# Kernel optimization log

Measured on AMD Instinct MI355X. Metric: run time of the kernel, lower is better.

The kernel has to match this reference:

```python
import jax, jax.numpy as jnp
import numpy as np

T = 512      # sequence length
D = 256      # char input dim
H = 512      # hidden dim
E = 256      # word embedding dim
V = 100000   # word alphabet size
KC = 2       # max skip-cells consumed per step
KP = 2       # max words starting per step
M = 340      # total lattice matches


def _build_gaz():
    # Deterministic lattice: at every 3rd position, two matched words of lengths 2 and 4.
    rng = np.random.default_rng(0)
    prod_word = np.zeros((T, KP), np.int32)
    prod_dest = np.full((T, KP), M, np.int32)   # default -> dummy slot
    prod_mask = np.zeros((T, KP), np.int32)
    cons_idx = np.zeros((T, KC), np.int32)
    cons_mask = np.zeros((T, KC), np.int32)
    cnt = np.zeros(T, np.int64)
    m = 0
    for t in range(0, T, 3):
        if t + 3 >= T:
            break
        for k, L in enumerate((2, 4)):
            e = t + L - 1  # end position where this word's cell is consumed
            prod_word[t, k] = rng.integers(0, V)
            prod_dest[t, k] = m
            prod_mask[t, k] = 1
            cons_idx[e, cnt[e]] = m
            cons_mask[e, cnt[e]] = 1
            cnt[e] += 1
            m += 1
    assert m == M
    return prod_word, prod_dest, prod_mask, cons_idx, cons_mask


def setup_inputs() -> dict:
    key = jax.random.key(0)
    ks = jax.random.split(key, 10)
    pw, pd, pm, ci, cm = _build_gaz()
    s = jnp.float32(0.05)
    return {
        "x": jax.random.normal(ks[0], (1, T, D), jnp.float32),
        "emb": jax.random.normal(ks[1], (V, E), jnp.float32) * s,
        "weight_ih": jax.random.normal(ks[2], (D, 3 * H), jnp.float32) * s,
        "weight_hh": jax.random.normal(ks[3], (H, 3 * H), jnp.float32) * s,
        "bias": jnp.zeros((3 * H,), jnp.float32),
        "alpha_weight_ih": jax.random.normal(ks[4], (D, H), jnp.float32) * s,
        "alpha_weight_hh": jax.random.normal(ks[5], (H, H), jnp.float32) * s,
        "alpha_bias": jnp.zeros((H,), jnp.float32),
        "w_weight_ih": jax.random.normal(ks[6], (E, 3 * H), jnp.float32) * s,
        "w_weight_hh": jax.random.normal(ks[7], (H, 3 * H), jnp.float32) * s,
        "w_bias": jnp.zeros((3 * H,), jnp.float32),
        "prod_word": jnp.asarray(pw),
        "prod_dest": jnp.asarray(pd),
        "prod_mask": jnp.asarray(pm),
        "cons_idx": jnp.asarray(ci),
        "cons_mask": jnp.asarray(cm),
        "num_matches": M,
    }


def _lattice_forward(x, emb, Wih, Whh, b, aWih, aWhh, ab, wWih, wWhh, wb,
                     prod_word, prod_dest, prod_mask, cons_idx, cons_mask, num_matches):
    Hd = Whh.shape[0]
    seq = jnp.transpose(x, (1, 0, 2))            # (T, 1, D) -- batch=1 as in original
    store0 = jnp.zeros((num_matches + 1, Hd), x.dtype)  # global skip-word cell store (+dummy)
    h0 = jnp.zeros((1, Hd), x.dtype)
    c0 = jnp.zeros((1, Hd), x.dtype)
    cmaskf = cons_mask.astype(x.dtype)           # (T, KC)
    pdest = jnp.where(prod_mask.astype(bool), prod_dest, num_matches)  # padded -> dummy slot

    def step(carry, inp):
        h, c, store = carry
        xt, cidx, cm, pw, pd = inp               # xt: (1,D)
        # MultiInputLSTMCell
        gates = xt @ Wih + h @ Whh + b           # (1, 3H)
        i, o, g = jnp.split(gates, 3, axis=1)
        i = jax.nn.sigmoid(i)
        o = jax.nn.sigmoid(o)
        g = jnp.tanh(g)
        c_in = store[cidx]                       # (KC, H) skip-word cell states ending here
        alpha = jnp.exp(jax.nn.sigmoid(xt @ aWih + ab + c_in @ aWhh)) * cm[:, None]
        ei = jnp.exp(i)                          # exp-normalize over [i; alpha] as in original
        denom = ei + alpha.sum(0, keepdims=True)
        c_skip = (g * ei + (c_in * alpha).sum(0, keepdims=True)) / denom
        c_plain = (1.0 - i) * c + i * g          # c_num == 0 branch
        c1 = jnp.where(cm.sum() > 0, c_skip, c_plain)
        h1 = o * jnp.tanh(c1)
        # WordLSTMCell for words starting at this position (dropout is identity in eval)
        we = emb[pw]                             # (KP, E)
        wg = we @ wWih + h1 @ wWhh + wb          # (KP, 3H)
        f2, i2, g2 = jnp.split(wg, 3, axis=1)
        ct = jax.nn.sigmoid(f2) * c1 + jax.nn.sigmoid(i2) * jnp.tanh(g2)  # (KP, H)
        store = store.at[pd].set(ct)             # padded rows write to dummy slot
        return (h1, c1, store), (h1[0], c1[0])

    (_, _, _), (hs, cs) = jax.lax.scan(
        step, (h0, c0, store0), (seq, cons_idx, cmaskf, prod_word, pdest))
    return hs[None], cs[None]                    # (1, T, H) each, like unsqueeze(0)


def reference(x, emb, weight_ih, weight_hh, bias, alpha_weight_ih, alpha_weight_hh,
              alpha_bias, w_weight_ih, w_weight_hh, w_bias,
              prod_word, prod_dest, prod_mask, cons_idx, cons_mask, num_matches):
    return _lattice_forward(x, emb, weight_ih, weight_hh, bias,
                            alpha_weight_ih, alpha_weight_hh, alpha_bias,
                            w_weight_ih, w_weight_hh, w_bias,
                            prod_word, prod_dest, prod_mask, cons_idx, cons_mask,
                            num_matches)
```

## Files before the change

### kernel.cpp

```cpp
#include <hip/hip_runtime.h>
#include <stdint.h>


#define T_LEN 512
#define H_DIM 512
#define G3    1536
#define NWG   32
#define NT    256
#define CH    16
#define SENTU 0xFFFFFFFFu
#define SCOPE_AGENT __HIP_MEMORY_SCOPE_AGENT

__device__ __forceinline__ float sigf(float x) { return 1.0f / (1.0f + __expf(-x)); }

#define REP32(F) F(0) F(1) F(2) F(3) F(4) F(5) F(6) F(7) F(8) F(9) F(10) F(11) \
                 F(12) F(13) F(14) F(15) F(16) F(17) F(18) F(19) F(20) F(21) F(22) \
                 F(23) F(24) F(25) F(26) F(27) F(28) F(29) F(30) F(31)

#define DECLW(u) float4 wA##u = {0.f,0.f,0.f,0.f}, wB##u = {0.f,0.f,0.f,0.f};

#define LDA1(u) wA##u = make_float4(srcA[(size_t)(ks4 + u*16 + 0) * ldA + gA],  \
                                    srcA[(size_t)(ks4 + u*16 + 1) * ldA + gA],  \
                                    srcA[(size_t)(ks4 + u*16 + 2) * ldA + gA],  \
                                    srcA[(size_t)(ks4 + u*16 + 3) * ldA + gA]);
#define LDB1(u) wB##u = make_float4(srcB[(size_t)(ks4 + u*16 + 0) * (size_t)G3 + gA], \
                                    srcB[(size_t)(ks4 + u*16 + 1) * (size_t)G3 + gA], \
                                    srcB[(size_t)(ks4 + u*16 + 2) * (size_t)G3 + gA], \
                                    srcB[(size_t)(ks4 + u*16 + 3) * (size_t)G3 + gA]);

#define DOTA1(u) { float4 hv = *(const float4*)&vecp[ks4 + u*16];                \
                   acc += hv.x*wA##u.x + hv.y*wA##u.y + hv.z*wA##u.z + hv.w*wA##u.w; }
#define DOTB1(u) { float4 hv = *(const float4*)&vecp[ks4 + u*16];                \
                   acc += hv.x*wB##u.x + hv.y*wB##u.y + hv.z*wB##u.z + hv.w*wB##u.w; }

#define RED4() do { acc += __shfl_down(acc, 2); acc += __shfl_down(acc, 1); } while (0)

__global__ __launch_bounds__(256) void proj_fused(
    const float* __restrict__ x, const float* __restrict__ Wih, const float* __restrict__ bias,
    const float* __restrict__ aWih, const float* __restrict__ ab,
    const float* __restrict__ emb, const float* __restrict__ wWih, const float* __restrict__ wb,
    const int* __restrict__ prod_word,
    float* __restrict__ Xg, float* __restrict__ Xa, float* __restrict__ Wgx) {
  const int b = blockIdx.x;
  const float *A, *W, *bi;
  float* out;
  const int* gather = nullptr;
  int rt, N, cb;
  if (b < 96)       { A = x;   W = Wih;  bi = bias; out = Xg;  N = 1536; rt = (b / 6) * 32;        cb = (b % 6) * 256; }
  else if (b < 128) { int bb = b - 96;  A = x;   W = aWih; bi = ab; out = Xa;  N = 512;  rt = (bb / 2) * 32; cb = (bb % 2) * 256; }
  else              { int bb = b - 128; A = emb; W = wWih; bi = wb; out = Wgx; N = 1536; gather = prod_word; rt = (bb / 6) * 32; cb = (bb % 6) * 256; }
  __shared__ float As[32][256];
  const int tid = threadIdx.x;
  for (int rr = 0; rr < 32; ++rr) {
    int r = rt + rr;
    int src = gather ? gather[r] : r;
    As[rr][tid] = A[(long)src * 256 + tid];
  }
  __syncthreads();
  const int c = cb + tid;
  float acc[32];
#pragma unroll
  for (int rr = 0; rr < 32; ++rr) acc[rr] = 0.f;
#pragma unroll 4
  for (int k = 0; k < 256; ++k) {
    float wv = W[(long)k * N + c];
#pragma unroll
    for (int rr = 0; rr < 32; ++rr) acc[rr] += As[rr][k] * wv;
  }
  float bv = bi[c];
  for (int rr = 0; rr < 32; ++rr) out[(long)(rt + rr) * N + c] = acc[rr] + bv;
}

__global__ __attribute__((amdgpu_flat_work_group_size(NT, NT), amdgpu_waves_per_eu(1, 1)))
void lattice_seq(
    const float* __restrict__ Whh,
    const float* __restrict__ aWhh,
    const float* __restrict__ wWhh,
    const float* __restrict__ Xg,
    const float* __restrict__ Xa,
    const float* __restrict__ Wgx,
    const int* __restrict__ prod_mask, const int* __restrict__ prod_dest,
    const int* __restrict__ cons_idx,  const int* __restrict__ cons_mask,
    float* __restrict__ Hbuf,
    float* __restrict__ store,
    float* __restrict__ out)
{
  const int tid = threadIdx.x;
  const int w = blockIdx.x;
  const int j0 = w * CH;
  float* outh = out;
  float* outc = out + (size_t)T_LEN * H_DIM;

  __shared__ float h1s[H_DIM];
  __shared__ float prevc1[CH];
  __shared__ float ds_g[3 * CH];
  __shared__ float ds_wg[3 * CH];
  __shared__ float ds_a[2 * CH];
  __shared__ float cins[2][H_DIM];
  __shared__ int l_pm[T_LEN * 2], l_pd[T_LEN * 2], l_ci[T_LEN * 2], l_cm[T_LEN * 2];

  for (int i = tid; i < T_LEN * 2; i += NT) {
    l_pm[i] = prod_mask[i];
    l_pd[i] = prod_dest[i];
    l_ci[i] = cons_idx[i];
    l_cm[i] = cons_mask[i];
  }

  int dcol, ks4;
  if (tid < 192) { dcol = tid >> 2; ks4 = (tid & 3) << 2; }
  else { int lane = tid - 192; dcol = lane >> 2; ks4 = (lane & 3) << 2; }

  REP32(DECLW)
  if (tid < 192) {
    const float* srcA = Whh;
    const float* srcB = wWhh;
    const size_t ldA = G3;
    const int gA = (dcol >> 4) * 512 + j0 + (dcol & 15);
    REP32(LDA1)
    REP32(LDB1)
  } else {
    const float* srcA = aWhh;
    const size_t ldA = H_DIM;
    const int gA = j0 + dcol;
    REP32(LDA1)
  }

  ((float2*)h1s)[tid] = make_float2(0.f, 0.f);
  if (tid < CH) prevc1[tid] = 0.f;
  __syncthreads();

  for (int e = 0; e < T_LEN; ++e) {
    const int p = e - 1;
    const bool prodp = (p >= 0) && ((l_pm[p * 2] | l_pm[p * 2 + 1]) != 0);
    const bool conse = (l_cm[e * 2] | l_cm[e * 2 + 1]) != 0;

    float xg0 = 0, xg1 = 0, xg2 = 0, xa0 = 0, wg0 = 0, wg1 = 0, wg2 = 0;
    if (tid < 16) {
      int j = j0 + tid;
      xg0 = Xg[(size_t)e * G3 + j];
      xg1 = Xg[(size_t)e * G3 + 512 + j];
      xg2 = Xg[(size_t)e * G3 + 1024 + j];
      xa0 = Xa[(size_t)e * H_DIM + j];
    }
    if (prodp && tid < 32) {
      int k = tid >> 4, jj = tid & 15, r = p * 2 + k;
      wg0 = Wgx[(size_t)r * G3 + j0 + jj];
      wg1 = Wgx[(size_t)r * G3 + 512 + j0 + jj];
      wg2 = Wgx[(size_t)r * G3 + 1024 + j0 + jj];
    }

    if (e > 0) {
      const unsigned long long* hrow =
          (const unsigned long long*)(Hbuf + (size_t)p * H_DIM);
      unsigned long long v;
      do {
        v = __hip_atomic_load(&hrow[tid], __ATOMIC_RELAXED, SCOPE_AGENT);
      } while ((unsigned)v == SENTU || (unsigned)(v >> 32) == SENTU);
      ((float2*)h1s)[tid] =
          make_float2(__uint_as_float((unsigned)v), __uint_as_float((unsigned)(v >> 32)));
    }
    __syncthreads();

    if (tid < 192) {
      const float* vecp = h1s;
      {
        float acc = 0.f;
        REP32(DOTA1)
        RED4();
        if ((tid & 3) == 0) ds_g[dcol] = acc;
      }
      if (prodp) {
        float acc = 0.f;
        REP32(DOTB1)
        RED4();
        if ((tid & 3) == 0) ds_wg[dcol] = acc;
      }
    }
    __syncthreads();

    if (prodp && tid < 32) {
      int k = tid >> 4, jj = tid & 15, r = p * 2 + k;
      if (l_pm[r]) {
        float f2 = wg0 + ds_wg[jj];
        float i2 = wg1 + ds_wg[16 + jj];
        float g2 = wg2 + ds_wg[32 + jj];
        float ct = sigf(f2) * prevc1[jj] + sigf(i2) * tanhf(g2);
        __hip_atomic_store(&store[(size_t)l_pd[r] * H_DIM + j0 + jj], ct,
                           __ATOMIC_RELAXED, SCOPE_AGENT);
      }
    }

    if (conse && tid >= 192) {
      const int lane = tid - 192;
      for (int k = 0; k < 2; ++k) {
        if (!l_cm[e * 2 + k]) continue;
        const size_t m = (size_t)l_ci[e * 2 + k];
        const unsigned long long* row2 = (const unsigned long long*)(store + m * H_DIM);
        float2* c2 = (float2*)&cins[k][0];
#pragma unroll
        for (int q = 0; q < 4; ++q) {
          unsigned long long v;
          do {
            v = __hip_atomic_load(&row2[q * 64 + lane], __ATOMIC_RELAXED, SCOPE_AGENT);
          } while ((unsigned)v == SENTU || (unsigned)(v >> 32) == SENTU);
          c2[q * 64 + lane] =
              make_float2(__uint_as_float((unsigned)v), __uint_as_float((unsigned)(v >> 32)));
        }
        asm volatile("s_waitcnt lgkmcnt(0)" ::: "memory");
        const float* vecp = &cins[k][0];
        float acc = 0.f;
        REP32(DOTA1)
        RED4();
        if ((lane & 3) == 0) ds_a[k * CH + dcol] = acc;
      }
    }
    if (conse) __syncthreads();

    if (tid < 16) {
      int j = j0 + tid;
      float ipre = xg0 + ds_g[tid];
      float opre = xg1 + ds_g[16 + tid];
      float gpre = xg2 + ds_g[32 + tid];
      float iv = sigf(ipre), ov = sigf(opre), gv = tanhf(gpre);
      float c1;
      if (conse) {
        float ei = __expf(iv);
        float asum = ei, csum = gv * ei;
#pragma unroll
        for (int k = 0; k < 2; ++k) {
          if (l_cm[e * 2 + k]) {
            float apre = xa0 + ds_a[k * CH + tid];
            float al = __expf(sigf(apre));
            asum += al;
            csum += cins[k][j] * al;
          }
        }
        c1 = csum / asum;
      } else {
        c1 = (1.f - iv) * prevc1[tid] + iv * gv;
      }
      float h1 = ov * tanhf(c1);
      prevc1[tid] = c1;
      __hip_atomic_store(&Hbuf[(size_t)e * H_DIM + j], h1, __ATOMIC_RELAXED, SCOPE_AGENT);
      outh[(size_t)e * H_DIM + j] = h1;
      outc[(size_t)e * H_DIM + j] = c1;
    }
  }
}

extern "C" void kernel_launch(void* const* d_in, const int* in_sizes, int n_in,
                              void* d_out, int out_size, void* d_ws, size_t ws_size,
                              hipStream_t stream) {
  const float* x    = (const float*)d_in[0];
  const float* emb  = (const float*)d_in[1];
  const float* Wih  = (const float*)d_in[2];
  const float* Whh  = (const float*)d_in[3];
  const float* bias = (const float*)d_in[4];
  const float* aWih = (const float*)d_in[5];
  const float* aWhh = (const float*)d_in[6];
  const float* ab   = (const float*)d_in[7];
  const float* wWih = (const float*)d_in[8];
  const float* wWhh = (const float*)d_in[9];
  const float* wb   = (const float*)d_in[10];
  const int* prod_word = (const int*)d_in[11];
  const int* prod_dest = (const int*)d_in[12];
  const int* prod_mask = (const int*)d_in[13];
  const int* cons_idx  = (const int*)d_in[14];
  const int* cons_mask = (const int*)d_in[15];

  float* ws    = (float*)d_ws;
  float* Xg    = ws;
  float* Xa    = Xg + 512 * 1536;
  float* Wgx   = Xa + 512 * 512;
  float* Hbuf  = Wgx + 1024 * 1536;
  float* store = Hbuf + 512 * 512;
  size_t need = ((size_t)512 * 1536 + 512 * 512 + 1024 * 1536 + 512 * 512 + 341 * 512) * 4;
  if (ws_size < need) return;

  hipMemsetAsync(Hbuf, 0xFF, (512 * 512 + 341 * 512) * sizeof(float), stream);

  proj_fused<<<dim3(320), dim3(256), 0, stream>>>(
      x, Wih, bias, aWih, ab, emb, wWih, wb, prod_word, Xg, Xa, Wgx);

  lattice_seq<<<dim3(NWG), dim3(NT), 0, stream>>>(
      Whh, aWhh, wWhh, Xg, Xa, Wgx,
      prod_mask, prod_dest, cons_idx, cons_mask,
      Hbuf, store, (float*)d_out);
}
```

Before: 2.311 ms.

## Restructure recurrent step to prefetch skip cells and overlap word-cell production

Reorganises the per-step schedule in the persistent lattice kernel. Skip-cell rows that were not produced in the previous step are staged into double-buffered shared memory before the hidden-state wait. The word-cell gate dot is computed first so its cell store can overlap with the main gate dot. Polling moves to inline-asm sc1 global loads with batched requests and a watchdog bound, and dot products use four independent accumulators to shorten FMA dependency chains. This adds extra barriers on production steps and a watchdog that could let sentinel values through if a producer stalls.

```diff
diff --git a/kernel.cpp b/kernel.cpp
--- a/kernel.cpp
+++ b/kernel.cpp
@@ -9,9 +9,40 @@
 #define NT    256
 #define CH    16
 #define SENTU 0xFFFFFFFFu
+#define WDOG  (1 << 17)
 #define SCOPE_AGENT __HIP_MEMORY_SCOPE_AGENT
 
+typedef unsigned u32x2 __attribute__((ext_vector_type(2)));
+typedef unsigned long long ull;
+
 __device__ __forceinline__ float sigf(float x) { return 1.0f / (1.0f + __expf(-x)); }
+
+__device__ __forceinline__ u32x2 mload8(const ull* p) {
+  u32x2 v;
+  asm volatile("global_load_dwordx2 %0, %1, off sc1\n\ts_waitcnt vmcnt(0)"
+               : "=v"(v) : "v"(p) : "memory");
+  return v;
+}
+__device__ __forceinline__ void mload8x2(const ull* p0, const ull* p1, u32x2& a, u32x2& b) {
+  asm volatile("global_load_dwordx2 %0, %2, off sc1\n\t"
+               "global_load_dwordx2 %1, %3, off sc1\n\t"
+               "s_waitcnt vmcnt(0)"
+               : "=&v"(a), "=&v"(b) : "v"(p0), "v"(p1) : "memory");
+}
+__device__ __forceinline__ void mload8x4(const ull* p0, const ull* p1, const ull* p2,
+                                         const ull* p3, u32x2& a, u32x2& b, u32x2& c, u32x2& d) {
+  asm volatile("global_load_dwordx2 %0, %4, off sc1\n\t"
+               "global_load_dwordx2 %1, %5, off sc1\n\t"
+               "global_load_dwordx2 %2, %6, off sc1\n\t"
+               "global_load_dwordx2 %3, %7, off sc1\n\t"
+               "s_waitcnt vmcnt(0)"
+               : "=&v"(a), "=&v"(b), "=&v"(c), "=&v"(d)
+               : "v"(p0), "v"(p1), "v"(p2), "v"(p3) : "memory");
+}
+__device__ __forceinline__ bool sent2(u32x2 v) { return v.x == SENTU || v.y == SENTU; }
+__device__ __forceinline__ float2 asf2(u32x2 v) {
+  return make_float2(__uint_as_float(v.x), __uint_as_float(v.y));
+}
 
 #define REP32(F) F(0) F(1) F(2) F(3) F(4) F(5) F(6) F(7) F(8) F(9) F(10) F(11) \
                  F(12) F(13) F(14) F(15) F(16) F(17) F(18) F(19) F(20) F(21) F(22) \
@@ -29,11 +60,39 @@
                                     srcB[(size_t)(ks4 + u*16 + 3) * (size_t)G3 + gA]);
 
 #define DOTA1(u) { float4 hv = *(const float4*)&vecp[ks4 + u*16];                \
-                   acc += hv.x*wA##u.x + hv.y*wA##u.y + hv.z*wA##u.z + hv.w*wA##u.w; }
+                   q.x += hv.x*wA##u.x; q.y += hv.y*wA##u.y;                     \
+                   q.z += hv.z*wA##u.z; q.w += hv.w*wA##u.w; }
 #define DOTB1(u) { float4 hv = *(const float4*)&vecp[ks4 + u*16];                \
-                   acc += hv.x*wB##u.x + hv.y*wB##u.y + hv.z*wB##u.z + hv.w*wB##u.w; }
-
-#define RED4() do { acc += __shfl_down(acc, 2); acc += __shfl_down(acc, 1); } while (0)
+                   q.x += hv.x*wB##u.x; q.y += hv.y*wB##u.y;                     \
+                   q.z += hv.z*wB##u.z; q.w += hv.w*wB##u.w; }
+#define DOT_FIN(dst, g) { float acc = (q.x + q.y) + (q.z + q.w);                 \
+                          acc += __shfl_down(acc, 2); acc += __shfl_down(acc, 1);\
+                          if (((g) & 3) == 0) dst = acc; }
+
+#define STAGE_ROW(k)  do {                                                       \
+    const size_t m_ = (size_t)l_ci[e * 2 + (k)];                                 \
+    const ull* row2_ = (const ull*)(store + m_ * H_DIM);                         \
+    u32x2 r0, r1, r2, r3;                                                        \
+    int gd_ = 0;                                                                 \
+    do {                                                                         \
+      mload8x4(row2_ + lane, row2_ + 64 + lane, row2_ + 128 + lane,              \
+               row2_ + 192 + lane, r0, r1, r2, r3);                              \
+    } while ((sent2(r0) || sent2(r1) || sent2(r2) || sent2(r3)) && ++gd_ < WDOG);\
+    float2* c2_ = (float2*)&cins[par][k][0];                                     \
+    c2_[lane] = asf2(r0);  c2_[64 + lane] = asf2(r1);                            \
+    c2_[128 + lane] = asf2(r2);  c2_[192 + lane] = asf2(r3);                     \
+  } while (0)
+
+#define ALPHA_DOT(k)  do {                                                       \
+    if (l_cm[e * 2 + (k)]) {                                                     \
+      asm volatile("s_waitcnt lgkmcnt(0)" ::: "memory");                         \
+      __builtin_amdgcn_sched_barrier(0);                                         \
+      const float* vecp = &cins[par][k][0];                                      \
+      float4 q = {0.f, 0.f, 0.f, 0.f};                                           \
+      REP32(DOTA1)                                                               \
+      DOT_FIN(ds_a[(k) * CH + dcol], lane)                                       \
+    }                                                                            \
+  } while (0)
 
 __global__ __launch_bounds__(256) void proj_fused(
     const float* __restrict__ x, const float* __restrict__ Wih, const float* __restrict__ bias,
@@ -73,12 +132,8 @@
 
 __global__ __attribute__((amdgpu_flat_work_group_size(NT, NT), amdgpu_waves_per_eu(1, 1)))
 void lattice_seq(
-    const float* __restrict__ Whh,
-    const float* __restrict__ aWhh,
-    const float* __restrict__ wWhh,
-    const float* __restrict__ Xg,
-    const float* __restrict__ Xa,
-    const float* __restrict__ Wgx,
+    const float* __restrict__ Whh, const float* __restrict__ aWhh, const float* __restrict__ wWhh,
+    const float* __restrict__ Xg, const float* __restrict__ Xa, const float* __restrict__ Wgx,
     const int* __restrict__ prod_mask, const int* __restrict__ prod_dest,
     const int* __restrict__ cons_idx,  const int* __restrict__ cons_mask,
     float* __restrict__ Hbuf,
@@ -96,7 +151,7 @@
   __shared__ float ds_g[3 * CH];
   __shared__ float ds_wg[3 * CH];
   __shared__ float ds_a[2 * CH];
-  __shared__ float cins[2][H_DIM];
+  __shared__ float cins[2][2][H_DIM];
   __shared__ int l_pm[T_LEN * 2], l_pd[T_LEN * 2], l_ci[T_LEN * 2], l_cm[T_LEN * 2];
 
   for (int i = tid; i < T_LEN * 2; i += NT) {
@@ -133,8 +188,16 @@
     const int p = e - 1;
     const bool prodp = (p >= 0) && ((l_pm[p * 2] | l_pm[p * 2 + 1]) != 0);
     const bool conse = (l_cm[e * 2] | l_cm[e * 2 + 1]) != 0;
-
-    float xg0 = 0, xg1 = 0, xg2 = 0, xa0 = 0, wg0 = 0, wg1 = 0, wg2 = 0;
+    const int par = e & 1;
+
+    bool fresh0 = false, fresh1 = false;
+    if (conse && prodp) {
+      int m0 = l_ci[e * 2], m1 = l_ci[e * 2 + 1];
+      fresh0 = (l_pm[p * 2] && l_pd[p * 2] == m0) || (l_pm[p * 2 + 1] && l_pd[p * 2 + 1] == m0);
+      fresh1 = (l_pm[p * 2] && l_pd[p * 2] == m1) || (l_pm[p * 2 + 1] && l_pd[p * 2 + 1] == m1);
+    }
+
+    float xg0 = 0, xg1 = 0, xg2 = 0, xa0 = 0;
     if (tid < 16) {
       int j = j0 + tid;
       xg0 = Xg[(size_t)e * G3 + j];
@@ -142,79 +205,87 @@
       xg2 = Xg[(size_t)e * G3 + 1024 + j];
       xa0 = Xa[(size_t)e * H_DIM + j];
     }
-    if (prodp && tid < 32) {
-      int k = tid >> 4, jj = tid & 15, r = p * 2 + k;
+    float wg0 = 0, wg1 = 0, wg2 = 0;
+    if (prodp && tid >= 192 && tid < 224) {
+      int lane = tid - 192, k = lane >> 4, jj = lane & 15, r = p * 2 + k;
       wg0 = Wgx[(size_t)r * G3 + j0 + jj];
       wg1 = Wgx[(size_t)r * G3 + 512 + j0 + jj];
       wg2 = Wgx[(size_t)r * G3 + 1024 + j0 + jj];
     }
 
-    if (e > 0) {
-      const unsigned long long* hrow =
-          (const unsigned long long*)(Hbuf + (size_t)p * H_DIM);
-      unsigned long long v;
-      do {
-        v = __hip_atomic_load(&hrow[tid], __ATOMIC_RELAXED, SCOPE_AGENT);
-      } while ((unsigned)v == SENTU || (unsigned)(v >> 32) == SENTU);
-      ((float2*)h1s)[tid] =
-          make_float2(__uint_as_float((unsigned)v), __uint_as_float((unsigned)(v >> 32)));
-    }
-    __syncthreads();
-
-    if (tid < 192) {
-      const float* vecp = h1s;
-      {
-        float acc = 0.f;
-        REP32(DOTA1)
-        RED4();
-        if ((tid & 3) == 0) ds_g[dcol] = acc;
-      }
-      if (prodp) {
-        float acc = 0.f;
-        REP32(DOTB1)
-        RED4();
-        if ((tid & 3) == 0) ds_wg[dcol] = acc;
-      }
-    }
-    __syncthreads();
-
-    if (prodp && tid < 32) {
-      int k = tid >> 4, jj = tid & 15, r = p * 2 + k;
-      if (l_pm[r]) {
-        float f2 = wg0 + ds_wg[jj];
-        float i2 = wg1 + ds_wg[16 + jj];
-        float g2 = wg2 + ds_wg[32 + jj];
-        float ct = sigf(f2) * prevc1[jj] + sigf(i2) * tanhf(g2);
-        __hip_atomic_store(&store[(size_t)l_pd[r] * H_DIM + j0 + jj], ct,
-                           __ATOMIC_RELAXED, SCOPE_AGENT);
-      }
-    }
-
     if (conse && tid >= 192) {
       const int lane = tid - 192;
-      for (int k = 0; k < 2; ++k) {
-        if (!l_cm[e * 2 + k]) continue;
-        const size_t m = (size_t)l_ci[e * 2 + k];
-        const unsigned long long* row2 = (const unsigned long long*)(store + m * H_DIM);
-        float2* c2 = (float2*)&cins[k][0];
-#pragma unroll
-        for (int q = 0; q < 4; ++q) {
-          unsigned long long v;
-          do {
-            v = __hip_atomic_load(&row2[q * 64 + lane], __ATOMIC_RELAXED, SCOPE_AGENT);
-          } while ((unsigned)v == SENTU || (unsigned)(v >> 32) == SENTU);
-          c2[q * 64 + lane] =
-              make_float2(__uint_as_float((unsigned)v), __uint_as_float((unsigned)(v >> 32)));
+      if (l_cm[e * 2] && !fresh0) STAGE_ROW(0);
+      if (l_cm[e * 2 + 1] && !fresh1) STAGE_ROW(1);
+    }
+
+    if (e > 0 && tid < 192) {
+      const ull* hrow = (const ull*)(Hbuf + (size_t)p * H_DIM);
+      if (tid < 64) {
+        u32x2 a, b;
+        int gd = 0;
+        do { mload8x2(hrow + tid, hrow + 192 + tid, a, b); }
+        while ((sent2(a) || sent2(b)) && ++gd < WDOG);
+        ((float2*)h1s)[tid] = asf2(a);
+        ((float2*)h1s)[192 + tid] = asf2(b);
+      } else {
+        u32x2 a;
+        int gd = 0;
+        do { a = mload8(hrow + tid); } while (sent2(a) && ++gd < WDOG);
+        ((float2*)h1s)[tid] = asf2(a);
+      }
+    }
+    __syncthreads();
+
+    if (prodp) {
+      if (tid < 192) {
+        const float* vecp = h1s;
+        float4 q = {0.f, 0.f, 0.f, 0.f};
+        REP32(DOTB1)
+        DOT_FIN(ds_wg[dcol], tid)
+      }
+      __syncthreads();
+      if (tid < 192) {
+        const float* vecp = h1s;
+        float4 q = {0.f, 0.f, 0.f, 0.f};
+        REP32(DOTA1)
+        DOT_FIN(ds_g[dcol], tid)
+      } else {
+        const int lane = tid - 192;
+        if (lane < 32) {
+          int k = lane >> 4, jj = lane & 15, r = p * 2 + k;
+          if (l_pm[r]) {
+            float f2 = wg0 + ds_wg[jj];
+            float i2 = wg1 + ds_wg[16 + jj];
+            float g2 = wg2 + ds_wg[32 + jj];
+            float ct = sigf(f2) * prevc1[jj] + sigf(i2) * tanhf(g2);
+            __hip_atomic_store(&store[(size_t)l_pd[r] * H_DIM + j0 + jj], ct,
+                               __ATOMIC_RELAXED, SCOPE_AGENT);
+          }
         }
-        asm volatile("s_waitcnt lgkmcnt(0)" ::: "memory");
-        const float* vecp = &cins[k][0];
-        float acc = 0.f;
+      }
+      __syncthreads();
+      if (conse && tid >= 192) {
+        const int lane = tid - 192;
+        if (l_cm[e * 2] && fresh0) STAGE_ROW(0);
+        if (l_cm[e * 2 + 1] && fresh1) STAGE_ROW(1);
+        ALPHA_DOT(0);
+        ALPHA_DOT(1);
+      }
+      __syncthreads();
+    } else {
+      if (tid < 192) {
+        const float* vecp = h1s;
+        float4 q = {0.f, 0.f, 0.f, 0.f};
         REP32(DOTA1)
-        RED4();
-        if ((lane & 3) == 0) ds_a[k * CH + dcol] = acc;
-      }
-    }
-    if (conse) __syncthreads();
+        DOT_FIN(ds_g[dcol], tid)
+      } else if (conse) {
+        const int lane = tid - 192;
+        ALPHA_DOT(0);
+        ALPHA_DOT(1);
+      }
+      __syncthreads();
+    }
 
     if (tid < 16) {
       int j = j0 + tid;
@@ -232,7 +303,7 @@
             float apre = xa0 + ds_a[k * CH + tid];
             float al = __expf(sigf(apre));
             asum += al;
-            csum += cins[k][j] * al;
+            csum += cins[par][k][j] * al;
           }
         }
         c1 = csum / asum;
```

Measured after the change: 2.009 ms. 13.1% less time.
